# Kernel optimization log

Measured on AMD Instinct MI355X. Metric: run time of the kernel, lower is better.

Reference implementation:

```python
import jax, jax.numpy as jnp
import numpy as np

N_NODES = 100000
N_EDGES = 3200000
IN_DIM = 128
OUT_DIM = 64
ITERS = 2


def setup_inputs() -> dict:
    key = jax.random.key(0)
    k1, k2, k3, k4, k5, k6 = jax.random.split(key, 6)
    feature = jax.random.normal(k1, (N_NODES, IN_DIM), dtype=jnp.float32)
    src = jax.random.randint(k2, (N_EDGES,), 0, N_NODES, dtype=jnp.int32)
    dst = jax.random.randint(k3, (N_EDGES,), 0, N_NODES, dtype=jnp.int32)
    # Kaiming-ish scaling for stability
    W_lin = jax.random.normal(k4, (IN_DIM, OUT_DIM), dtype=jnp.float32) / np.sqrt(IN_DIM)
    W_d1 = jax.random.normal(k5, (OUT_DIM, OUT_DIM), dtype=jnp.float32) / np.sqrt(OUT_DIM)
    W_d2 = jax.random.normal(k6, (OUT_DIM, OUT_DIM), dtype=jnp.float32) / np.sqrt(OUT_DIM)
    return {"feature": feature, "src": src, "dst": dst,
            "W_lin": W_lin, "W_d1": W_d1, "W_d2": W_d2}


def reference(feature, src, dst, W_lin, W_d1, W_d2):
    # u_i^0 = 0 ; u_i^j = tanh(linear(x_i) + dense(sum_{k in N(i)} u_k^{j-1}))
    base = feature @ W_lin                       # [N, OUT_DIM] (no bias)
    n = feature.shape[0]
    u = jnp.zeros((n, OUT_DIM), dtype=feature.dtype)
    for _ in range(ITERS):
        # copy_u + sum: message u[src] scattered-summed at dst
        m = jax.ops.segment_sum(u[src], dst, num_segments=n)   # [N, OUT_DIM]
        # Dense (2 layers, relu between, no bias): W_d2 @ relu(W_d1 @ m)
        h = jax.nn.relu(m @ W_d1) @ W_d2
        u = jnp.tanh(base + h)
    return u
```

## Files before the change

### kernel.cpp

```cpp
#include <hip/hip_runtime.h>
#include <math.h>

#define N_NODES 100000
#define N_EDGES 3200000
#define IN_DIM  128
#define OUT_DIM 64

#define BSHIFT   7
#define BNODES   128
#define NBUCKETS ((N_NODES + BNODES - 1) / BNODES)
#define NBINBLK  1024
#define CHUNK    (N_EDGES / NBINBLK)
#define SEGCAP   6144
#define MTILES   (N_NODES / 16)
#define GEMM_BLOCKS ((MTILES + 3) / 4)

typedef _Float16 half8 __attribute__((ext_vector_type(8)));
typedef float    f32x4 __attribute__((ext_vector_type(4)));

__device__ __forceinline__ int xcd_swz(int i) {
    return (i & 7) * (NBINBLK / 8) + (i >> 3);
}

__device__ __forceinline__ void scan_btot(
    const int* __restrict__ Btot, int* bs, int* tmp)
{
    int t = threadIdx.x;
    const int C = (NBUCKETS + 511) / 512;
    int b0 = t * C;
    int s = 0;
#pragma unroll
    for (int i = 0; i < C; ++i) {
        int idx = b0 + i;
        int v = (idx < NBUCKETS) ? Btot[idx] : 0;
        if (idx < NBUCKETS) bs[idx] = v;
        s += v;
    }
    tmp[t] = s;
    __syncthreads();
#pragma unroll
    for (int o = 1; o < 512; o <<= 1) {
        int v = (t >= o) ? tmp[t - o] : 0;
        __syncthreads();
        tmp[t] += v;
        __syncthreads();
    }
    int excl = (t == 0) ? 0 : tmp[t - 1];
#pragma unroll
    for (int i = 0; i < C; ++i) {
        int idx = b0 + i;
        if (idx < NBUCKETS) { int v = bs[idx]; bs[idx] = excl; excl += v; }
    }
    __syncthreads();
}

__global__ __launch_bounds__(256) void fused_gemm_hist(
    const float* __restrict__ feature,
    const float* __restrict__ Wlin,
    float* __restrict__ base,
    _Float16* __restrict__ u1h,
    const int* __restrict__ dst,
    int* __restrict__ H)
{
    __shared__ int h[NBUCKETS];

    if (blockIdx.x < NBINBLK) {
        for (int k = threadIdx.x; k < NBUCKETS; k += 256) h[k] = 0;
        __syncthreads();

        int b = xcd_swz(blockIdx.x);
        int beg = b * CHUNK, end = beg + CHUNK;
        for (int i = beg + threadIdx.x; i < end; i += 256)
            atomicAdd(&h[dst[i] >> BSHIFT], 1);
        __syncthreads();

        for (int k = threadIdx.x; k < NBUCKETS; k += 256)
            H[(size_t)k * NBINBLK + b] = h[k];
        return;
    }

    int lane = threadIdx.x & 63;
    int wid  = ((blockIdx.x - NBINBLK) * 256 + threadIdx.x) >> 6;
    if (wid >= MTILES) return;

    int mrow = lane & 15;
    int kb   = lane >> 4;
    int k0   = kb * 8;

    half8 b[4][4];
#pragma unroll
    for (int s = 0; s < 4; ++s)
#pragma unroll
        for (int n = 0; n < 4; ++n)
#pragma unroll
            for (int j = 0; j < 8; ++j)
                b[s][n][j] = (_Float16)Wlin[(s * 32 + k0 + j) * OUT_DIM + n * 16 + mrow];

    int row = wid * 16 + mrow;
    const float4* fr = reinterpret_cast<const float4*>(feature + (size_t)row * IN_DIM);
    half8 a[4];
#pragma unroll
    for (int s = 0; s < 4; ++s) {
        float4 lo = fr[(s * 32 + k0) >> 2];
        float4 hi = fr[((s * 32 + k0) >> 2) + 1];
        a[s][0] = (_Float16)lo.x; a[s][1] = (_Float16)lo.y;
        a[s][2] = (_Float16)lo.z; a[s][3] = (_Float16)lo.w;
        a[s][4] = (_Float16)hi.x; a[s][5] = (_Float16)hi.y;
        a[s][6] = (_Float16)hi.z; a[s][7] = (_Float16)hi.w;
    }

    f32x4 acc[4];
#pragma unroll
    for (int n = 0; n < 4; ++n) acc[n] = (f32x4)0.f;

#pragma unroll
    for (int s = 0; s < 4; ++s)
#pragma unroll
        for (int n = 0; n < 4; ++n)
            acc[n] = __builtin_amdgcn_mfma_f32_16x16x32_f16(a[s], b[s][n], acc[n], 0, 0, 0);

#pragma unroll
    for (int n = 0; n < 4; ++n)
#pragma unroll
        for (int j = 0; j < 4; ++j) {
            int r = wid * 16 + kb * 4 + j;
            int c = n * 16 + mrow;
            float v = acc[n][j];
            base[(size_t)r * OUT_DIM + c] = v;
            u1h[(size_t)r * OUT_DIM + c] = (_Float16)tanhf(v);
        }
}

__global__ __launch_bounds__(NBINBLK) void scan_local(
    int* __restrict__ H, int* __restrict__ Btot)
{
    __shared__ int s[NBINBLK];
    int k = blockIdx.x, t = threadIdx.x;
    int v = H[(size_t)k * NBINBLK + t];
    s[t] = v;
    __syncthreads();
#pragma unroll
    for (int off = 1; off < NBINBLK; off <<= 1) {
        int x = (t >= off) ? s[t - off] : 0;
        __syncthreads();
        s[t] += x;
        __syncthreads();
    }
    H[(size_t)k * NBINBLK + t] = s[t] - v;
    if (t == NBINBLK - 1) Btot[k] = s[t];
}

__global__ __launch_bounds__(512) void bin_scatter(
    const int* __restrict__ src,
    const int* __restrict__ dst,
    const int* __restrict__ H,
    const int* __restrict__ Btot,
    int* __restrict__ ebuf)
{
    __shared__ int cur[NBUCKETS];
    __shared__ int bs[NBUCKETS];
    __shared__ int tmp[512];

    scan_btot(Btot, bs, tmp);

    int b = xcd_swz(blockIdx.x);
    for (int k = threadIdx.x; k < NBUCKETS; k += 512)
        cur[k] = H[(size_t)k * NBINBLK + b] + bs[k];
    __syncthreads();

    int beg = b * CHUNK, end = beg + CHUNK;
    for (int i = beg + threadIdx.x; i < end; i += 512) {
        int d = dst[i];
        int k = d >> BSHIFT;
        int p = atomicAdd(&cur[k], 1);
        ebuf[p] = src[i] | ((d & (BNODES - 1)) << 17);
    }
}

__global__ __launch_bounds__(512) void bucket_sort(
    const int* __restrict__ Btot,
    int* __restrict__ ebuf,
    int* __restrict__ node_off)
{
    __shared__ int seg[SEGCAP];
    __shared__ int cnt[BNODES];
    __shared__ int off[BNODES];
    __shared__ int bs[NBUCKETS];
    __shared__ int tmp[512];

    scan_btot(Btot, bs, tmp);

    int k = blockIdx.x;
    int beg = bs[k];
    int end = (k + 1 < NBUCKETS) ? bs[k + 1] : N_EDGES;
    int n = end - beg;

    for (int j = threadIdx.x; j < BNODES; j += 512) cnt[j] = 0;
    __syncthreads();

    for (int i = threadIdx.x; i < n; i += 512) {
        int v = ebuf[beg + i];
        seg[i] = v;
        atomicAdd(&cnt[v >> 17], 1);
    }
    __syncthreads();

    if (threadIdx.x == 0) {
        int node0 = k * BNODES;
        int nvalid = N_NODES - node0; if (nvalid > BNODES) nvalid = BNODES;
        int excl = 0;
        for (int j = 0; j < nvalid; ++j) {
            off[j] = excl;
            node_off[node0 + j] = beg + excl;
            excl += cnt[j];
        }
        if (k == NBUCKETS - 1) node_off[N_NODES] = end;
    }
    __syncthreads();

    for (int i = threadIdx.x; i < n; i += 512) {
        int v = seg[i];
        int p = atomicAdd(&off[v >> 17], 1);
        ebuf[beg + p] = v & 0x1FFFF;
    }
}

__global__ __launch_bounds__(256) void node_gather(
    const int* __restrict__ node_off,
    const int* __restrict__ csr,
    const half8* __restrict__ u1v,
    half8* __restrict__ mh)
{
    int wid = (blockIdx.x * 256 + threadIdx.x) >> 6;
    if (wid >= N_NODES) return;
    int lane = threadIdx.x & 63;
    int q = lane >> 3, c = lane & 7;

    int beg = node_off[wid];
    int end = node_off[wid + 1];
    int cnt = end - beg;
    int per = (cnt + 7) >> 3;
    int gb  = beg + q * per;
    int ge  = gb + per; if (ge > end) ge = end;

    float acc[8];
#pragma unroll
    for (int i = 0; i < 8; ++i) acc[i] = 0.f;

    int e = gb;
    for (; e + 4 <= ge; e += 4) {
        int s0 = csr[e];
        int s1 = csr[e + 1];
        int s2 = csr[e + 2];
        int s3 = csr[e + 3];
        half8 a = u1v[(size_t)s0 * 8 + c];
        half8 b = u1v[(size_t)s1 * 8 + c];
        half8 g = u1v[(size_t)s2 * 8 + c];
        half8 d = u1v[(size_t)s3 * 8 + c];
#pragma unroll
        for (int i = 0; i < 8; ++i)
            acc[i] += ((float)a[i] + (float)b[i]) + ((float)g[i] + (float)d[i]);
    }
    for (; e < ge; ++e) {
        half8 a = u1v[(size_t)csr[e] * 8 + c];
#pragma unroll
        for (int i = 0; i < 8; ++i) acc[i] += (float)a[i];
    }

#pragma unroll
    for (int i = 0; i < 8; ++i) {
        acc[i] += __shfl_xor(acc[i], 8);
        acc[i] += __shfl_xor(acc[i], 16);
        acc[i] += __shfl_xor(acc[i], 32);
    }

    if (q == 0) {
        half8 hv;
#pragma unroll
        for (int i = 0; i < 8; ++i) hv[i] = (_Float16)acc[i];
        mh[(size_t)wid * 8 + c] = hv;
    }
}

__global__ __launch_bounds__(256) void dense_tanh(
    const half8* __restrict__ mh,
    const float* __restrict__ W1,
    const float* __restrict__ W2,
    const float* __restrict__ base,
    float* __restrict__ out)
{
    __shared__ _Float16 tl[4][16][72];
    int lane = threadIdx.x & 63;
    int w    = threadIdx.x >> 6;
    int wid  = (blockIdx.x * 256 + threadIdx.x) >> 6;
    if (wid >= MTILES) return;

    int mrow = lane & 15;
    int kb   = lane >> 4;
    int k0   = kb * 8;

    half8 b1[2][4], b2[2][4];
#pragma unroll
    for (int s = 0; s < 2; ++s)
#pragma unroll
        for (int n = 0; n < 4; ++n)
#pragma unroll
            for (int j = 0; j < 8; ++j) {
                b1[s][n][j] = (_Float16)W1[(s * 32 + k0 + j) * 64 + n * 16 + mrow];
                b2[s][n][j] = (_Float16)W2[(s * 32 + k0 + j) * 64 + n * 16 + mrow];
            }

    int row = wid * 16 + mrow;
    half8 a[2];
#pragma unroll
    for (int s = 0; s < 2; ++s)
        a[s] = mh[(size_t)row * 8 + ((s * 32 + k0) >> 3)];

    f32x4 acc1[4];
#pragma unroll
    for (int n = 0; n < 4; ++n) acc1[n] = (f32x4)0.f;
#pragma unroll
    for (int s = 0; s < 2; ++s)
#pragma unroll
        for (int n = 0; n < 4; ++n)
            acc1[n] = __builtin_amdgcn_mfma_f32_16x16x32_f16(a[s], b1[s][n], acc1[n], 0, 0, 0);

#pragma unroll
    for (int n = 0; n < 4; ++n)
#pragma unroll
        for (int j = 0; j < 4; ++j)
            tl[w][kb * 4 + j][n * 16 + mrow] = (_Float16)fmaxf(acc1[n][j], 0.f);

    half8 a2[2];
#pragma unroll
    for (int s = 0; s < 2; ++s)
        a2[s] = *reinterpret_cast<const half8*>(&tl[w][mrow][s * 32 + k0]);

    f32x4 acc2[4];
#pragma unroll
    for (int n = 0; n < 4; ++n) acc2[n] = (f32x4)0.f;
#pragma unroll
    for (int s = 0; s < 2; ++s)
#pragma unroll
        for (int n = 0; n < 4; ++n)
            acc2[n] = __builtin_amdgcn_mfma_f32_16x16x32_f16(a2[s], b2[s][n], acc2[n], 0, 0, 0);

#pragma unroll
    for (int n = 0; n < 4; ++n)
#pragma unroll
        for (int j = 0; j < 4; ++j) {
            int r = wid * 16 + kb * 4 + j;
            int c = n * 16 + mrow;
            out[(size_t)r * 64 + c] = tanhf(base[(size_t)r * 64 + c] + acc2[n][j]);
        }
}

extern "C" void kernel_launch(void* const* d_in, const int* in_sizes, int n_in,
                              void* d_out, int out_size, void* d_ws, size_t ws_size,
                              hipStream_t stream)
{
    const float* feature = (const float*)d_in[0];
    const int*   src     = (const int*)d_in[1];
    const int*   dst     = (const int*)d_in[2];
    const float* W_lin   = (const float*)d_in[3];
    const float* W_d1    = (const float*)d_in[4];
    const float* W_d2    = (const float*)d_in[5];
    float* out = (float*)d_out;

    const size_t NODE_F = (size_t)N_NODES * OUT_DIM;

    float*    base     = (float*)d_ws;
    _Float16* u1h      = (_Float16*)(base + NODE_F);
    _Float16* mh       = u1h + NODE_F;
    int*      H        = (int*)(mh + NODE_F);
    int*      Btot     = H + ((size_t)NBUCKETS * NBINBLK + 4);
    int*      node_off = Btot + (NBUCKETS + 4);
    int*      ebuf     = node_off + (N_NODES + 4);

    fused_gemm_hist<<<NBINBLK + GEMM_BLOCKS, 256, 0, stream>>>(
        feature, W_lin, base, u1h, dst, H);

    scan_local<<<NBUCKETS, NBINBLK, 0, stream>>>(H, Btot);
    bin_scatter<<<NBINBLK, 512, 0, stream>>>(src, dst, H, Btot, ebuf);
    bucket_sort<<<NBUCKETS, 512, 0, stream>>>(Btot, ebuf, node_off);

    int gather_blocks = (int)(((size_t)N_NODES * 64 + 255) / 256);
    node_gather<<<gather_blocks, 256, 0, stream>>>(
        node_off, ebuf, (const half8*)u1h, (half8*)mh);

    dense_tanh<<<GEMM_BLOCKS, 256, 0, stream>>>(
        (const half8*)mh, W_d1, W_d2, base, out);
}
```

Measured before the change: 157.4 us.

## Fuse bucket sort with neighbor gather using LDS-resident sorted edges

Merges the per-bucket counting sort and the per-node gather-sum into one kernel. The sorted source indices stay in shared memory instead of being written back to the edge buffer and reread, and the node offset array is dropped along with one kernel launch. Each 512-thread block now gathers for its 128 nodes, one 8-lane group per node, with no intra-node split across lanes, which may reduce parallelism per node. Edges are staged in registers up to a fixed per-bucket capacity, so buckets larger than SEGCAP would be silently truncated.

New measurement: 140.5 us. 1.12x faster.

```diff
diff --git a/kernel.cpp b/kernel.cpp
--- a/kernel.cpp
+++ b/kernel.cpp
@@ -14,6 +14,7 @@
 #define SEGCAP   6144
 #define MTILES   (N_NODES / 16)
 #define GEMM_BLOCKS ((MTILES + 3) / 4)
+#define RSTAGE   (SEGCAP / 512)
 
 typedef _Float16 half8 __attribute__((ext_vector_type(8)));
 typedef float    f32x4 __attribute__((ext_vector_type(4)));
@@ -177,14 +178,16 @@
     }
 }
 
-__global__ __launch_bounds__(512) void bucket_sort(
+__global__ __launch_bounds__(512) void sort_gather(
     const int* __restrict__ Btot,
-    int* __restrict__ ebuf,
-    int* __restrict__ node_off)
+    const int* __restrict__ ebuf,
+    const half8* __restrict__ u1v,
+    half8* __restrict__ mh)
 {
     __shared__ int seg[SEGCAP];
     __shared__ int cnt[BNODES];
     __shared__ int off[BNODES];
+    __shared__ int st[BNODES + 1];
     __shared__ int bs[NBUCKETS];
     __shared__ int tmp[512];
 
@@ -198,87 +201,74 @@
     for (int j = threadIdx.x; j < BNODES; j += 512) cnt[j] = 0;
     __syncthreads();
 
-    for (int i = threadIdx.x; i < n; i += 512) {
-        int v = ebuf[beg + i];
-        seg[i] = v;
-        atomicAdd(&cnt[v >> 17], 1);
+    int r[RSTAGE];
+#pragma unroll
+    for (int it = 0; it < RSTAGE; ++it) {
+        int i = threadIdx.x + it * 512;
+        int v = (i < n) ? ebuf[beg + i] : -1;
+        r[it] = v;
+        if (v >= 0) atomicAdd(&cnt[v >> 17], 1);
     }
     __syncthreads();
 
     if (threadIdx.x == 0) {
-        int node0 = k * BNODES;
-        int nvalid = N_NODES - node0; if (nvalid > BNODES) nvalid = BNODES;
         int excl = 0;
-        for (int j = 0; j < nvalid; ++j) {
-            off[j] = excl;
-            node_off[node0 + j] = beg + excl;
-            excl += cnt[j];
-        }
-        if (k == NBUCKETS - 1) node_off[N_NODES] = end;
-    }
-    __syncthreads();
-
-    for (int i = threadIdx.x; i < n; i += 512) {
-        int v = seg[i];
-        int p = atomicAdd(&off[v >> 17], 1);
-        ebuf[beg + p] = v & 0x1FFFF;
-    }
-}
-
-__global__ __launch_bounds__(256) void node_gather(
-    const int* __restrict__ node_off,
-    const int* __restrict__ csr,
-    const half8* __restrict__ u1v,
-    half8* __restrict__ mh)
-{
-    int wid = (blockIdx.x * 256 + threadIdx.x) >> 6;
-    if (wid >= N_NODES) return;
-    int lane = threadIdx.x & 63;
-    int q = lane >> 3, c = lane & 7;
-
-    int beg = node_off[wid];
-    int end = node_off[wid + 1];
-    int cnt = end - beg;
-    int per = (cnt + 7) >> 3;
-    int gb  = beg + q * per;
-    int ge  = gb + per; if (ge > end) ge = end;
-
-    float acc[8];
-#pragma unroll
-    for (int i = 0; i < 8; ++i) acc[i] = 0.f;
-
-    int e = gb;
-    for (; e + 4 <= ge; e += 4) {
-        int s0 = csr[e];
-        int s1 = csr[e + 1];
-        int s2 = csr[e + 2];
-        int s3 = csr[e + 3];
-        half8 a = u1v[(size_t)s0 * 8 + c];
-        half8 b = u1v[(size_t)s1 * 8 + c];
-        half8 g = u1v[(size_t)s2 * 8 + c];
-        half8 d = u1v[(size_t)s3 * 8 + c];
-#pragma unroll
-        for (int i = 0; i < 8; ++i)
-            acc[i] += ((float)a[i] + (float)b[i]) + ((float)g[i] + (float)d[i]);
-    }
-    for (; e < ge; ++e) {
-        half8 a = u1v[(size_t)csr[e] * 8 + c];
-#pragma unroll
-        for (int i = 0; i < 8; ++i) acc[i] += (float)a[i];
-    }
-
-#pragma unroll
-    for (int i = 0; i < 8; ++i) {
-        acc[i] += __shfl_xor(acc[i], 8);
-        acc[i] += __shfl_xor(acc[i], 16);
-        acc[i] += __shfl_xor(acc[i], 32);
-    }
-
-    if (q == 0) {
+        for (int j = 0; j < BNODES; ++j) {
+            st[j] = excl; off[j] = excl; excl += cnt[j];
+        }
+        st[BNODES] = excl;
+    }
+    __syncthreads();
+
+#pragma unroll
+    for (int it = 0; it < RSTAGE; ++it) {
+        int v = r[it];
+        if (v >= 0) {
+            int p = atomicAdd(&off[v >> 17], 1);
+            seg[p] = v & 0x1FFFF;
+        }
+    }
+    __syncthreads();
+
+    int g = threadIdx.x >> 3;
+    int c = threadIdx.x & 7;
+    int node0 = k * BNODES;
+
+#pragma unroll
+    for (int half = 0; half < 2; ++half) {
+        int j = g + half * 64;
+        int node = node0 + j;
+        if (node >= N_NODES) break;
+        int eb = st[j], ee = st[j + 1];
+
+        float acc[8];
+#pragma unroll
+        for (int i = 0; i < 8; ++i) acc[i] = 0.f;
+
+        int e = eb;
+        for (; e + 4 <= ee; e += 4) {
+            int s0 = seg[e];
+            int s1 = seg[e + 1];
+            int s2 = seg[e + 2];
+            int s3 = seg[e + 3];
+            half8 a = u1v[(size_t)s0 * 8 + c];
+            half8 b = u1v[(size_t)s1 * 8 + c];
+            half8 gg = u1v[(size_t)s2 * 8 + c];
+            half8 d = u1v[(size_t)s3 * 8 + c];
+#pragma unroll
+            for (int i = 0; i < 8; ++i)
+                acc[i] += ((float)a[i] + (float)b[i]) + ((float)gg[i] + (float)d[i]);
+        }
+        for (; e < ee; ++e) {
+            half8 a = u1v[(size_t)seg[e] * 8 + c];
+#pragma unroll
+            for (int i = 0; i < 8; ++i) acc[i] += (float)a[i];
+        }
+
         half8 hv;
 #pragma unroll
         for (int i = 0; i < 8; ++i) hv[i] = (_Float16)acc[i];
-        mh[(size_t)wid * 8 + c] = hv;
+        mh[(size_t)node * 8 + c] = hv;
     }
 }
 
@@ -374,19 +364,15 @@
     _Float16* mh       = u1h + NODE_F;
     int*      H        = (int*)(mh + NODE_F);
     int*      Btot     = H + ((size_t)NBUCKETS * NBINBLK + 4);
-    int*      node_off = Btot + (NBUCKETS + 4);
-    int*      ebuf     = node_off + (N_NODES + 4);
+    int*      ebuf     = Btot + (NBUCKETS + 4);
 
     fused_gemm_hist<<<NBINBLK + GEMM_BLOCKS, 256, 0, stream>>>(
         feature, W_lin, base, u1h, dst, H);
 
     scan_local<<<NBUCKETS, NBINBLK, 0, stream>>>(H, Btot);
     bin_scatter<<<NBINBLK, 512, 0, stream>>>(src, dst, H, Btot, ebuf);
-    bucket_sort<<<NBUCKETS, 512, 0, stream>>>(Btot, ebuf, node_off);
-
-    int gather_blocks = (int)(((size_t)N_NODES * 64 + 255) / 256);
-    node_gather<<<gather_blocks, 256, 0, stream>>>(
-        node_off, ebuf, (const half8*)u1h, (half8*)mh);
+    sort_gather<<<NBUCKETS, 512, 0, stream>>>(
+        Btot, ebuf, (const half8*)u1h, (half8*)mh);
 
     dense_tanh<<<GEMM_BLOCKS, 256, 0, stream>>>(
         (const half8*)mh, W_d1, W_d2, base, out);
```
